# Performance work log

Hardware: AMD Instinct MI355X
Metric: run time of the kernel (lower is better)

## Reference

```python
import jax, jax.numpy as jnp
import numpy as np

DIM, HEADS, DFF = 768, 12, 3072
DK = DIM // HEADS
EPS = 1e-5

def _layernorm(x, w, b):
    mu = jnp.mean(x, axis=-1, keepdims=True)
    var = jnp.mean(jnp.square(x - mu), axis=-1, keepdims=True)
    return (x - mu) * jax.lax.rsqrt(var + EPS) * w + b

def setup_inputs() -> dict:
    key = jax.random.key(0)
    ks = jax.random.split(key, 5)
    B, N = 8, 1024
    std = 0.02
    return {
        "x": jax.random.normal(ks[0], (B, N, DIM), jnp.float32),
        "ln1_w": jnp.ones((DIM,), jnp.float32),
        "ln1_b": jnp.zeros((DIM,), jnp.float32),
        "qkv_w": jax.random.normal(ks[1], (3 * DIM, DIM), jnp.float32) * std,
        "qkv_b": jnp.zeros((3 * DIM,), jnp.float32),
        "proj_w": jax.random.normal(ks[2], (DIM, DIM), jnp.float32) * std,
        "proj_b": jnp.zeros((DIM,), jnp.float32),
        "ln2_w": jnp.ones((DIM,), jnp.float32),
        "ln2_b": jnp.zeros((DIM,), jnp.float32),
        "fc1_w": jax.random.normal(ks[3], (DFF, DIM), jnp.float32) * std,
        "fc1_b": jnp.zeros((DFF,), jnp.float32),
        "fc2_w": jax.random.normal(ks[4], (DIM, DFF), jnp.float32) * std,
        "fc2_b": jnp.zeros((DIM,), jnp.float32),
    }

def reference(x, ln1_w, ln1_b, qkv_w, qkv_b, proj_w, proj_b,
              ln2_w, ln2_b, fc1_w, fc1_b, fc2_w, fc2_b):
    B, N, C = x.shape
    # --- attention branch (pre-norm) ---
    h = _layernorm(x, ln1_w, ln1_b)
    qkv = h @ qkv_w.T + qkv_b                      # [B,N,3C]
    qkv = qkv.reshape(B, N, 3, HEADS, DK)
    q = qkv[:, :, 0].transpose(0, 2, 1, 3)         # [B,H,N,dk]
    k = qkv[:, :, 1].transpose(0, 2, 1, 3)
    v = qkv[:, :, 2].transpose(0, 2, 1, 3)
    scale = DK ** -0.5
    attn = jnp.einsum('bhnd,bhmd->bhnm', q, k) * scale
    attn = jax.nn.softmax(attn, axis=-1)
    out = jnp.einsum('bhnm,bhmd->bhnd', attn, v)   # [B,H,N,dk]
    out = out.transpose(0, 2, 1, 3).reshape(B, N, C)
    out = out @ proj_w.T + proj_b
    x = x + out
    # --- MLP branch (pre-norm) ---
    h = _layernorm(x, ln2_w, ln2_b)
    h = jax.nn.gelu(h @ fc1_w.T + fc1_b, approximate=False)
    h = h @ fc2_w.T + fc2_b
    return x + h
```

## Files before the change

kernel.cpp:

```cpp
#include <hip/hip_runtime.h>
#include <hip/hip_bf16.h>
#include <hip/hip_fp8.h>
#include <math.h>

typedef __attribute__((ext_vector_type(8))) __bf16 bf16x8;
typedef __attribute__((ext_vector_type(4))) __bf16 bf16x4;
typedef __attribute__((ext_vector_type(4))) float f32x4;
typedef __attribute__((ext_vector_type(4))) int i32x4;
typedef __attribute__((ext_vector_type(8))) int i32x8;

#define DIM 768
#define DFF 3072
#define HEADS 12
#define DKH 64
#define SEQ 1024
#define BATCH 8
#define ROWS (SEQ * BATCH)

#define GLD16(gp, lp)                                                      \
  __builtin_amdgcn_global_load_lds(                                        \
      (const __attribute__((address_space(1))) void*)(gp),                 \
      (__attribute__((address_space(3))) void*)(lp), 16, 0, 0)

__device__ __forceinline__ unsigned int pack4_e4m3(float a, float b, float c, float d) {
  __hip_fp8_e4m3 q0(a), q1(b), q2(c), q3(d);
  return (unsigned int)q0.__x | ((unsigned int)q1.__x << 8) |
         ((unsigned int)q2.__x << 16) | ((unsigned int)q3.__x << 24);
}

__global__ __launch_bounds__(256) void cvt4_kernel(const float* __restrict__ s0, int n0,
                                                   const float* __restrict__ s1, int n1,
                                                   const float* __restrict__ s2, int n2,
                                                   const float* __restrict__ s3, int n3,
                                                   __bf16* __restrict__ d0,
                                                   __bf16* __restrict__ d1,
                                                   unsigned char* __restrict__ d2,
                                                   unsigned char* __restrict__ d3) {
  int i0 = blockIdx.x * 256 + threadIdx.x;
  int st = gridDim.x * 256;
  const float* bsrc[2] = {s0, s1};
  __bf16* bdst[2] = {d0, d1};
  int bns[2] = {n0, n1};
#pragma unroll
  for (int t = 0; t < 2; ++t) {
    const f32x4* in = reinterpret_cast<const f32x4*>(bsrc[t]);
    bf16x4* out = reinterpret_cast<bf16x4*>(bdst[t]);
    for (int i = i0; i < bns[t]; i += st) {
      f32x4 v = in[i];
      bf16x4 o;
#pragma unroll
      for (int j = 0; j < 4; ++j) o[j] = (__bf16)v[j];
      out[i] = o;
    }
  }
  const float* fsrc[2] = {s2, s3};
  unsigned char* fdst[2] = {d2, d3};
  int fns[2] = {n2, n3};
#pragma unroll
  for (int t = 0; t < 2; ++t) {
    const f32x4* in = reinterpret_cast<const f32x4*>(fsrc[t]);
    unsigned int* out = reinterpret_cast<unsigned int*>(fdst[t]);
    for (int i = i0; i < fns[t]; i += st) {
      f32x4 v = in[i];
      out[i] = pack4_e4m3(v[0] * 16.f, v[1] * 16.f, v[2] * 16.f, v[3] * 16.f);
    }
  }
}

__global__ __launch_bounds__(256) void ln_kernel(const float* __restrict__ x,
                                                 const float* __restrict__ w,
                                                 const float* __restrict__ b,
                                                 __bf16* __restrict__ out) {
  int wid = threadIdx.x >> 6, lane = threadIdx.x & 63;
  int row = blockIdx.x * 4 + wid;
  const f32x4* xp = reinterpret_cast<const f32x4*>(x + (size_t)row * DIM);
  f32x4 v[3];
  float s1 = 0.f, s2 = 0.f;
#pragma unroll
  for (int i = 0; i < 3; ++i) {
    v[i] = xp[lane + i * 64];
#pragma unroll
    for (int c = 0; c < 4; ++c) { s1 += v[i][c]; s2 += v[i][c] * v[i][c]; }
  }
#pragma unroll
  for (int off = 1; off < 64; off <<= 1) {
    s1 += __shfl_xor(s1, off, 64);
    s2 += __shfl_xor(s2, off, 64);
  }
  float mu = s1 * (1.f / DIM);
  float var = s2 * (1.f / DIM) - mu * mu;
  float rs = rsqrtf(var + 1e-5f);
  const f32x4* wp = reinterpret_cast<const f32x4*>(w);
  const f32x4* bp = reinterpret_cast<const f32x4*>(b);
  __bf16* op = out + (size_t)row * DIM;
#pragma unroll
  for (int i = 0; i < 3; ++i) {
    int c4 = lane + i * 64;
    f32x4 wv = wp[c4], bv = bp[c4];
    bf16x4 ov;
#pragma unroll
    for (int c = 0; c < 4; ++c) ov[c] = (__bf16)((v[i][c] - mu) * rs * wv[c] + bv[c]);
    *reinterpret_cast<bf16x4*>(&op[c4 * 4]) = ov;
  }
}

__global__ __launch_bounds__(256) void ln_f8_kernel(const float* __restrict__ x,
                                                    const float* __restrict__ w,
                                                    const float* __restrict__ b,
                                                    unsigned char* __restrict__ out) {
  int wid = threadIdx.x >> 6, lane = threadIdx.x & 63;
  int row = blockIdx.x * 4 + wid;
  const f32x4* xp = reinterpret_cast<const f32x4*>(x + (size_t)row * DIM);
  f32x4 v[3];
  float s1 = 0.f, s2 = 0.f;
#pragma unroll
  for (int i = 0; i < 3; ++i) {
    v[i] = xp[lane + i * 64];
#pragma unroll
    for (int c = 0; c < 4; ++c) { s1 += v[i][c]; s2 += v[i][c] * v[i][c]; }
  }
#pragma unroll
  for (int off = 1; off < 64; off <<= 1) {
    s1 += __shfl_xor(s1, off, 64);
    s2 += __shfl_xor(s2, off, 64);
  }
  float mu = s1 * (1.f / DIM);
  float var = s2 * (1.f / DIM) - mu * mu;
  float rs = rsqrtf(var + 1e-5f);
  const f32x4* wp = reinterpret_cast<const f32x4*>(w);
  const f32x4* bp = reinterpret_cast<const f32x4*>(b);
  unsigned int* op = reinterpret_cast<unsigned int*>(out + (size_t)row * DIM);
#pragma unroll
  for (int i = 0; i < 3; ++i) {
    int c4 = lane + i * 64;
    f32x4 wv = wp[c4], bv = bp[c4];
    float o0 = (v[i][0] - mu) * rs * wv[0] + bv[0];
    float o1 = (v[i][1] - mu) * rs * wv[1] + bv[1];
    float o2 = (v[i][2] - mu) * rs * wv[2] + bv[2];
    float o3 = (v[i][3] - mu) * rs * wv[3] + bv[3];
    op[c4] = pack4_e4m3(o0, o1, o2, o3);
  }
}

template <int EPI, int BN, int DBUF>
__global__ __launch_bounds__(256, 3) void gemm_nt(const __bf16* __restrict__ A,
                                                  const __bf16* __restrict__ B,
                                                  const float* __restrict__ bias,
                                                  const float* __restrict__ resid,
                                                  __bf16* __restrict__ vt,
                                                  void* __restrict__ Cout,
                                                  int M, int N, int K) {
  constexpr int NBUF = DBUF ? 2 : 1;
  constexpr int MF = (BN == 128) ? 4 : 2;
  static_assert(BN == 64, "vmcnt count assumes 6 staging loads per thread");
  __shared__ __bf16 As[NBUF * 128 * 64];
  __shared__ __bf16 Bs[NBUF * BN * 64];
  int tid = threadIdx.x;
  int bm = blockIdx.x, bn = blockIdx.y;
  int wid = tid >> 6, lane = tid & 63;
  int l15 = lane & 15, l4 = lane >> 4;
  int rowb = (BN == 128) ? (wid >> 1) * 64 : wid * 32;
  int colb = (BN == 128) ? (wid & 1) * 64 : 0;

  f32x4 acc[MF][4] = {};

  auto stage = [&](int buf, int kt) {
    __bf16* Ab = As + buf * 128 * 64;
    __bf16* Bb = Bs + buf * BN * 64;
#pragma unroll
    for (int r = 0; r < 4; ++r) {
      int c0 = (r * 4 + wid) * 64;
      int c = c0 + lane;
      int row = c >> 3;
      int colE = ((c & 7) ^ (row & 7)) * 8;
      GLD16(&A[(size_t)(bm * 128 + row) * K + kt + colE], &Ab[c0 * 8]);
    }
#pragma unroll
    for (int r = 0; r < BN / 32; ++r) {
      int c0 = (r * 4 + wid) * 64;
      int c = c0 + lane;
      int row = c >> 3;
      int colE = ((c & 7) ^ (row & 7)) * 8;
      GLD16(&B[(size_t)(bn * BN + row) * K + kt + colE], &Bb[c0 * 8]);
    }
  };

  auto compute = [&](int buf) {
    const __bf16* Ab = As + buf * 128 * 64;
    const __bf16* Bb = Bs + buf * BN * 64;
#pragma unroll
    for (int kc = 0; kc < 2; ++kc) {
      int cswz = ((kc * 4 + l4) ^ (l15 & 7)) * 8;
      bf16x8 af[MF], bfr[4];
#pragma unroll
      for (int m = 0; m < MF; ++m)
        af[m] = *reinterpret_cast<const bf16x8*>(&Ab[(rowb + m * 16 + l15) * 64 + cswz]);
#pragma unroll
      for (int n = 0; n < 4; ++n)
        bfr[n] = *reinterpret_cast<const bf16x8*>(&Bb[(colb + n * 16 + l15) * 64 + cswz]);
#pragma unroll
      for (int m = 0; m < MF; ++m)
#pragma unroll
        for (int n = 0; n < 4; ++n)
          acc[m][n] = __builtin_amdgcn_mfma_f32_16x16x32_bf16(af[m], bfr[n], acc[m][n], 0, 0, 0);
    }
  };

  if constexpr (DBUF) {
    stage(0, 0);
    int cur = 0;
    for (int kt = 0; kt < K; kt += 64) {
      if (kt + 64 < K) {
        stage(cur ^ 1, kt + 64);
        asm volatile("s_waitcnt vmcnt(6)" ::: "memory");
      } else {
        asm volatile("s_waitcnt vmcnt(0)" ::: "memory");
      }
      __builtin_amdgcn_s_barrier();
      compute(cur);
      asm volatile("s_waitcnt lgkmcnt(0)" ::: "memory");
      __builtin_amdgcn_s_barrier();
      cur ^= 1;
    }
  } else {
    for (int kt = 0; kt < K; kt += 64) {
      __syncthreads();
      stage(0, kt);
      __syncthreads();
      compute(0);
    }
  }

#pragma unroll
  for (int m = 0; m < MF; ++m)
#pragma unroll
    for (int n = 0; n < 4; ++n) {
      int row0 = bm * 128 + rowb + m * 16 + l4 * 4;
      int col = bn * BN + colb + n * 16 + l15;
      float bc = bias[col];
      if (EPI == 0 && col >= 2 * DIM) {
        int h = (col - 2 * DIM) >> 6, dk = (col - 2 * DIM) & 63;
        int b = row0 >> 10, tok = row0 & 1023;
        bf16x4 pk;
#pragma unroll
        for (int j = 0; j < 4; ++j) pk[j] = (__bf16)(acc[m][n][j] + bc);
        *reinterpret_cast<bf16x4*>(
            &vt[(size_t)((b * HEADS + h) * DKH + dk) * SEQ + tok]) = pk;
      } else {
#pragma unroll
        for (int j = 0; j < 4; ++j) {
          float v = acc[m][n][j] + bc;
          size_t idx = (size_t)(row0 + j) * N + col;
          if (EPI == 0) {
            ((__bf16*)Cout)[idx] = (__bf16)v;
          } else {
            ((float*)Cout)[idx] = v + resid[idx];
          }
        }
      }
    }
}

template <int EPI>
__global__ __launch_bounds__(256, 3) void gemm_fp8(const unsigned char* __restrict__ A,
                                                   const unsigned char* __restrict__ B,
                                                   const float* __restrict__ bias,
                                                   const float* __restrict__ resid,
                                                   void* __restrict__ Cout,
                                                   int M, int N, int K) {
  __shared__ unsigned char As[2 * 128 * 128];
  __shared__ unsigned char Bs[2 * 64 * 128];
  int tid = threadIdx.x;
  int bm = blockIdx.x, bn = blockIdx.y;
  int wid = tid >> 6, lane = tid & 63;
  int l15 = lane & 15, l4 = lane >> 4;
  int rowb = wid * 32;

  f32x4 acc[2][4] = {};

  auto stage = [&](int buf, int kt) {
    unsigned char* Ab = As + buf * 128 * 128;
    unsigned char* Bb = Bs + buf * 64 * 128;
#pragma unroll
    for (int r = 0; r < 4; ++r) {
      int c0 = (r * 4 + wid) * 64;
      int c = c0 + lane;
      int row = c >> 3;
      int j = (c & 7) ^ (row & 7);
      GLD16(&A[(size_t)(bm * 128 + row) * K + kt + j * 16], &Ab[c0 * 16]);
    }
#pragma unroll
    for (int r = 0; r < 2; ++r) {
      int c0 = (r * 4 + wid) * 64;
      int c = c0 + lane;
      int row = c >> 3;
      int j = (c & 7) ^ (row & 7);
      GLD16(&B[(size_t)(bn * 64 + row) * K + kt + j * 16], &Bb[c0 * 16]);
    }
  };

  auto ld32 = [&](const unsigned char* base, int row) -> i32x8 {
    int s7 = l15 & 7;
    i32x8 r;
    *reinterpret_cast<i32x4*>(&r) =
        *reinterpret_cast<const i32x4*>(&base[row * 128 + (((2 * l4) ^ s7) * 16)]);
    *(reinterpret_cast<i32x4*>(&r) + 1) =
        *reinterpret_cast<const i32x4*>(&base[row * 128 + (((2 * l4 + 1) ^ s7) * 16)]);
    return r;
  };

  auto compute = [&](int buf) {
    const unsigned char* Ab = As + buf * 128 * 128;
    const unsigned char* Bb = Bs + buf * 64 * 128;
    i32x8 af[2], bfr[4];
#pragma unroll
    for (int m = 0; m < 2; ++m) af[m] = ld32(Ab, rowb + m * 16 + l15);
#pragma unroll
    for (int n = 0; n < 4; ++n) bfr[n] = ld32(Bb, n * 16 + l15);
#pragma unroll
    for (int m = 0; m < 2; ++m)
#pragma unroll
      for (int n = 0; n < 4; ++n)
        acc[m][n] = __builtin_amdgcn_mfma_scale_f32_16x16x128_f8f6f4(
            af[m], bfr[n], acc[m][n], 0, 0,
            0, 0x7F7F7F7F,
            0, 0x7F7F7F7F);
  };

  stage(0, 0);
  int cur = 0;
  for (int kt = 0; kt < K; kt += 128) {
    if (kt + 128 < K) {
      stage(cur ^ 1, kt + 128);
      asm volatile("s_waitcnt vmcnt(6)" ::: "memory");
    } else {
      asm volatile("s_waitcnt vmcnt(0)" ::: "memory");
    }
    __builtin_amdgcn_s_barrier();
    compute(cur);
    asm volatile("s_waitcnt lgkmcnt(0)" ::: "memory");
    __builtin_amdgcn_s_barrier();
    cur ^= 1;
  }

#pragma unroll
  for (int m = 0; m < 2; ++m)
#pragma unroll
    for (int n = 0; n < 4; ++n) {
      int row0 = bm * 128 + rowb + m * 16 + l4 * 4;
      int col = bn * 64 + n * 16 + l15;
      float bc = bias[col];
#pragma unroll
      for (int j = 0; j < 4; ++j) {
        if (EPI == 0) {
          float v = acc[m][n][j] * 0.0625f + bc;
          float z = 1.59576912f * (v + 0.044715f * v * v * v);
          float tt = __expf(fminf(z, 80.f));
          float g = v * __fdividef(tt, tt + 1.0f);
          ((unsigned char*)Cout)[(size_t)(row0 + j) * N + col] =
              __hip_fp8_e4m3(g * 16.f).__x;
        } else {
          size_t idx = (size_t)(row0 + j) * N + col;
          ((float*)Cout)[idx] = acc[m][n][j] * (1.f / 256.f) + bc + resid[idx];
        }
      }
    }
}

__global__ __launch_bounds__(256, 3) void attn_kernel(const __bf16* __restrict__ qkv,
                                                      const __bf16* __restrict__ vt,
                                                      __bf16* __restrict__ out) {
  int bid = blockIdx.x;
  int xcd = bid & 7, kk0 = bid >> 3;
  int bh = (kk0 >> 3) * 8 + xcd;
  int qt = kk0 & 7;
  int b = bh / HEADS, h = bh % HEADS;
  int tid = threadIdx.x, wid = tid >> 6, lane = tid & 63;
  int l15 = lane & 15, l4 = lane >> 4;
  int qr0 = qt * 128 + wid * 32;
  const size_t rs = 3 * DIM;
  const __bf16* Qb = qkv + (size_t)(b * SEQ) * rs + h * DKH;
  const __bf16* Kb = Qb + DIM;
  const __bf16* Vb = vt + (size_t)bh * DKH * SEQ;

  __shared__ __bf16 Ks[64 * 64];
  __shared__ __bf16 Vs[64 * 64];
  __shared__ __bf16 Ps[4][32][72];
  __bf16(*Psw)[72] = Ps[wid];

  bf16x8 qf[2][2];
#pragma unroll
  for (int m = 0; m < 2; ++m)
#pragma unroll
    for (int kc = 0; kc < 2; ++kc) {
      bf16x8 t = *reinterpret_cast<const bf16x8*>(
          &Qb[(size_t)(qr0 + m * 16 + l15) * rs + kc * 32 + l4 * 8]);
#pragma unroll
      for (int e = 0; e < 8; ++e) t[e] = (__bf16)((float)t[e] * 0.125f);
      qf[m][kc] = t;
    }

  f32x4 o[2][4] = {};
  f32x4 lsum[2] = {};

  for (int kv0 = 0; kv0 < SEQ; kv0 += 64) {
    __syncthreads();
#pragma unroll
    for (int cc = 0; cc < 2; ++cc) {
      int c0 = (wid * 2 + cc) * 64;
      int c = c0 + lane;
      int row = c >> 3;
      int sb = (c & 7) * 16;
      int pkc = sb ^ (((row >> 2) & 7) << 4);
      GLD16(&Kb[(size_t)(kv0 + row) * rs + (pkc >> 1)], &Ks[c0 * 8]);
      int pvc = sb ^ ((row & 7) << 4);
      GLD16(&Vb[(size_t)row * SEQ + kv0 + (pvc >> 1)], &Vs[c0 * 8]);
    }
    __syncthreads();

    bf16x8 kb[4][2];
#pragma unroll
    for (int nf = 0; nf < 4; ++nf)
#pragma unroll
      for (int kc = 0; kc < 2; ++kc) {
        int row = 4 * l15 + nf;
        int col = (kc * 64 + l4 * 16) ^ ((l15 & 7) << 4);
        kb[nf][kc] = *reinterpret_cast<const bf16x8*>(&Ks[row * 64 + (col >> 1)]);
      }
    f32x4 s[2][4] = {};
#pragma unroll
    for (int m = 0; m < 2; ++m)
#pragma unroll
      for (int nf = 0; nf < 4; ++nf)
#pragma unroll
        for (int kc = 0; kc < 2; ++kc)
          s[m][nf] = __builtin_amdgcn_mfma_f32_16x16x32_bf16(qf[m][kc], kb[nf][kc], s[m][nf], 0, 0, 0);

    bf16x8 vf[4][2];
#pragma unroll
    for (int d = 0; d < 4; ++d)
#pragma unroll
      for (int kc = 0; kc < 2; ++kc) {
        int row = d * 16 + l15;
        int col = (kc * 64 + l4 * 16) ^ ((l15 & 7) << 4);
        vf[d][kc] = *reinterpret_cast<const bf16x8*>(&Vs[row * 64 + (col >> 1)]);
      }

#pragma unroll
    for (int m = 0; m < 2; ++m)
#pragma unroll
      for (int j = 0; j < 4; ++j) {
        bf16x4 pk;
        float ss = 0.f;
#pragma unroll
        for (int nf = 0; nf < 4; ++nf) {
          float p = __expf(s[m][nf][j]);
          ss += p;
          pk[nf] = (__bf16)p;
        }
        lsum[m][j] += ss;
        *reinterpret_cast<bf16x4*>(&Psw[m * 16 + l4 * 4 + j][l15 * 4]) = pk;
      }
    asm volatile("s_waitcnt lgkmcnt(0)" ::: "memory");
    __builtin_amdgcn_sched_barrier(0);

    bf16x8 pf[2][2];
#pragma unroll
    for (int m = 0; m < 2; ++m)
#pragma unroll
      for (int kc = 0; kc < 2; ++kc)
        pf[m][kc] = *reinterpret_cast<const bf16x8*>(&Psw[m * 16 + l15][kc * 32 + l4 * 8]);
#pragma unroll
    for (int m = 0; m < 2; ++m)
#pragma unroll
      for (int d = 0; d < 4; ++d)
#pragma unroll
        for (int kc = 0; kc < 2; ++kc)
          o[m][d] = __builtin_amdgcn_mfma_f32_16x16x32_bf16(pf[m][kc], vf[d][kc], o[m][d], 0, 0, 0);
  }

#pragma unroll
  for (int off = 1; off < 16; off <<= 1)
#pragma unroll
    for (int m = 0; m < 2; ++m)
#pragma unroll
      for (int j = 0; j < 4; ++j) lsum[m][j] += __shfl_xor(lsum[m][j], off, 64);

  __bf16* op = out + (size_t)(b * SEQ) * DIM + h * DKH;
#pragma unroll
  for (int m = 0; m < 2; ++m)
#pragma unroll
    for (int j = 0; j < 4; ++j) {
      float rl = 1.f / lsum[m][j];
      int row = qr0 + m * 16 + l4 * 4 + j;
#pragma unroll
      for (int d = 0; d < 4; ++d)
        op[(size_t)row * DIM + d * 16 + l15] = (__bf16)(o[m][d][j] * rl);
    }
}

extern "C" void kernel_launch(void* const* d_in, const int* in_sizes, int n_in,
                              void* d_out, int out_size, void* d_ws, size_t ws_size,
                              hipStream_t stream) {
  const float* x      = (const float*)d_in[0];
  const float* ln1_w  = (const float*)d_in[1];
  const float* ln1_b  = (const float*)d_in[2];
  const float* qkv_w  = (const float*)d_in[3];
  const float* qkv_b  = (const float*)d_in[4];
  const float* proj_w = (const float*)d_in[5];
  const float* proj_b = (const float*)d_in[6];
  const float* ln2_w  = (const float*)d_in[7];
  const float* ln2_b  = (const float*)d_in[8];
  const float* fc1_w  = (const float*)d_in[9];
  const float* fc1_b  = (const float*)d_in[10];
  const float* fc2_w  = (const float*)d_in[11];
  const float* fc2_b  = (const float*)d_in[12];

  char* ws = (char*)d_ws;
  size_t o = 0;
  __bf16* qkvw_bf = (__bf16*)(ws + o); o += (size_t)3 * DIM * DIM * 2;
  __bf16* projw_bf = (__bf16*)(ws + o); o += (size_t)DIM * DIM * 2;
  unsigned char* fc1w_f8 = (unsigned char*)(ws + o); o += (size_t)DFF * DIM;
  unsigned char* fc2w_f8 = (unsigned char*)(ws + o); o += (size_t)DIM * DFF;
  __bf16* h_bf    = (__bf16*)(ws + o); o += (size_t)ROWS * DIM * 2;
  float*  x1      = (float*)(ws + o);  o += (size_t)ROWS * DIM * 4;
  __bf16* qkv_bf  = (__bf16*)(ws + o); o += (size_t)ROWS * 3 * DIM * 2;
  __bf16* attn_bf = (__bf16*)(ws + o); o += (size_t)ROWS * DIM * 2;
  unsigned char* ff_f8 = (unsigned char*)qkv_bf;
  __bf16* vtp     = (__bf16*)x1;
  unsigned char* h_f8 = (unsigned char*)h_bf;

  cvt4_kernel<<<2048, 256, 0, stream>>>(
      qkv_w, 3 * DIM * DIM / 4, proj_w, DIM * DIM / 4,
      fc1_w, DFF * DIM / 4, fc2_w, DIM * DFF / 4,
      qkvw_bf, projw_bf, fc1w_f8, fc2w_f8);

  ln_kernel<<<ROWS / 4, 256, 0, stream>>>(x, ln1_w, ln1_b, h_bf);
  gemm_nt<0, 64, 1><<<dim3(ROWS / 128, 3 * DIM / 64), 256, 0, stream>>>(
      h_bf, qkvw_bf, qkv_b, nullptr, vtp, qkv_bf, ROWS, 3 * DIM, DIM);
  attn_kernel<<<dim3(8 * BATCH * HEADS), 256, 0, stream>>>(qkv_bf, vtp, attn_bf);
  gemm_nt<2, 64, 1><<<dim3(ROWS / 128, DIM / 64), 256, 0, stream>>>(
      attn_bf, projw_bf, proj_b, x, nullptr, x1, ROWS, DIM, DIM);
  ln_f8_kernel<<<ROWS / 4, 256, 0, stream>>>(x1, ln2_w, ln2_b, h_f8);
  gemm_fp8<0><<<dim3(ROWS / 128, DFF / 64), 256, 0, stream>>>(
      h_f8, fc1w_f8, fc1_b, nullptr, ff_f8, ROWS, DFF, DIM);
  gemm_fp8<1><<<dim3(ROWS / 128, DIM / 64), 256, 0, stream>>>(
      ff_f8, fc2w_f8, fc2_b, x1, (float*)d_out, ROWS, DIM, DFF);
}
```

Measured before the change: 193.5 us.

## Widen GEMM tiles to 128x128 with 8 waves per block

```diff
diff --git a/kernel.cpp b/kernel.cpp
--- a/kernel.cpp
+++ b/kernel.cpp
@@ -142,101 +142,89 @@
   }
 }
 
-template <int EPI, int BN, int DBUF>
-__global__ __launch_bounds__(256, 3) void gemm_nt(const __bf16* __restrict__ A,
+template <int EPI>
+__global__ __launch_bounds__(512, 4) void gemm_nt(const __bf16* __restrict__ A,
                                                   const __bf16* __restrict__ B,
                                                   const float* __restrict__ bias,
                                                   const float* __restrict__ resid,
                                                   __bf16* __restrict__ vt,
                                                   void* __restrict__ Cout,
                                                   int M, int N, int K) {
-  constexpr int NBUF = DBUF ? 2 : 1;
-  constexpr int MF = (BN == 128) ? 4 : 2;
-  static_assert(BN == 64, "vmcnt count assumes 6 staging loads per thread");
-  __shared__ __bf16 As[NBUF * 128 * 64];
-  __shared__ __bf16 Bs[NBUF * BN * 64];
+  __shared__ __bf16 As[2 * 128 * 64];
+  __shared__ __bf16 Bs[2 * 128 * 64];
   int tid = threadIdx.x;
   int bm = blockIdx.x, bn = blockIdx.y;
   int wid = tid >> 6, lane = tid & 63;
   int l15 = lane & 15, l4 = lane >> 4;
-  int rowb = (BN == 128) ? (wid >> 1) * 64 : wid * 32;
-  int colb = (BN == 128) ? (wid & 1) * 64 : 0;
-
-  f32x4 acc[MF][4] = {};
+  int rowb = (wid >> 1) * 32;
+  int colb = (wid & 1) * 64;
+
+  f32x4 acc[2][4] = {};
 
   auto stage = [&](int buf, int kt) {
     __bf16* Ab = As + buf * 128 * 64;
-    __bf16* Bb = Bs + buf * BN * 64;
-#pragma unroll
-    for (int r = 0; r < 4; ++r) {
-      int c0 = (r * 4 + wid) * 64;
+    __bf16* Bb = Bs + buf * 128 * 64;
+#pragma unroll
+    for (int r = 0; r < 2; ++r) {
+      int c0 = (r * 8 + wid) * 64;
       int c = c0 + lane;
       int row = c >> 3;
       int colE = ((c & 7) ^ (row & 7)) * 8;
       GLD16(&A[(size_t)(bm * 128 + row) * K + kt + colE], &Ab[c0 * 8]);
     }
 #pragma unroll
-    for (int r = 0; r < BN / 32; ++r) {
-      int c0 = (r * 4 + wid) * 64;
+    for (int r = 0; r < 2; ++r) {
+      int c0 = (r * 8 + wid) * 64;
       int c = c0 + lane;
       int row = c >> 3;
       int colE = ((c & 7) ^ (row & 7)) * 8;
-      GLD16(&B[(size_t)(bn * BN + row) * K + kt + colE], &Bb[c0 * 8]);
+      GLD16(&B[(size_t)(bn * 128 + row) * K + kt + colE], &Bb[c0 * 8]);
     }
   };
 
   auto compute = [&](int buf) {
     const __bf16* Ab = As + buf * 128 * 64;
-    const __bf16* Bb = Bs + buf * BN * 64;
+    const __bf16* Bb = Bs + buf * 128 * 64;
 #pragma unroll
     for (int kc = 0; kc < 2; ++kc) {
       int cswz = ((kc * 4 + l4) ^ (l15 & 7)) * 8;
-      bf16x8 af[MF], bfr[4];
-#pragma unroll
-      for (int m = 0; m < MF; ++m)
+      bf16x8 af[2], bfr[4];
+#pragma unroll
+      for (int m = 0; m < 2; ++m)
         af[m] = *reinterpret_cast<const bf16x8*>(&Ab[(rowb + m * 16 + l15) * 64 + cswz]);
 #pragma unroll
       for (int n = 0; n < 4; ++n)
         bfr[n] = *reinterpret_cast<const bf16x8*>(&Bb[(colb + n * 16 + l15) * 64 + cswz]);
 #pragma unroll
-      for (int m = 0; m < MF; ++m)
+      for (int m = 0; m < 2; ++m)
 #pragma unroll
         for (int n = 0; n < 4; ++n)
           acc[m][n] = __builtin_amdgcn_mfma_f32_16x16x32_bf16(af[m], bfr[n], acc[m][n], 0, 0, 0);
     }
   };
 
-  if constexpr (DBUF) {
-    stage(0, 0);
-    int cur = 0;
-    for (int kt = 0; kt < K; kt += 64) {
-      if (kt + 64 < K) {
-        stage(cur ^ 1, kt + 64);
-        asm volatile("s_waitcnt vmcnt(6)" ::: "memory");
-      } else {
-        asm volatile("s_waitcnt vmcnt(0)" ::: "memory");
-      }
-      __builtin_amdgcn_s_barrier();
-      compute(cur);
-      asm volatile("s_waitcnt lgkmcnt(0)" ::: "memory");
-      __builtin_amdgcn_s_barrier();
-      cur ^= 1;
-    }
-  } else {
-    for (int kt = 0; kt < K; kt += 64) {
-      __syncthreads();
-      stage(0, kt);
-      __syncthreads();
-      compute(0);
-    }
-  }
-
-#pragma unroll
-  for (int m = 0; m < MF; ++m)
+  stage(0, 0);
+  int cur = 0;
+  for (int kt = 0; kt < K; kt += 64) {
+    if (kt + 64 < K) {
+      stage(cur ^ 1, kt + 64);
+      asm volatile("s_waitcnt vmcnt(4)" ::: "memory");
+    } else {
+      asm volatile("s_waitcnt vmcnt(0)" ::: "memory");
+    }
+    __builtin_amdgcn_s_barrier();
+    compute(cur);
+    asm volatile("s_waitcnt lgkmcnt(0)" ::: "memory");
+    __builtin_amdgcn_s_barrier();
+    cur ^= 1;
+  }
+
+#pragma unroll
+  for (int m = 0; m < 2; ++m)
 #pragma unroll
     for (int n = 0; n < 4; ++n) {
       int row0 = bm * 128 + rowb + m * 16 + l4 * 4;
-      int col = bn * BN + colb + n * 16 + l15;
+      int col = bn * 128 + colb + n * 16 + l15;
       float bc = bias[col];
       if (EPI == 0 && col >= 2 * DIM) {
         int h = (col - 2 * DIM) >> 6, dk = (col - 2 * DIM) & 63;
@@ -262,28 +250,29 @@
 }
 
 template <int EPI>
-__global__ __launch_bounds__(256, 3) void gemm_fp8(const unsigned char* __restrict__ A,
+__global__ __launch_bounds__(512, 4) void gemm_fp8(const unsigned char* __restrict__ A,
                                                    const unsigned char* __restrict__ B,
                                                    const float* __restrict__ bias,
                                                    const float* __restrict__ resid,
                                                    void* __restrict__ Cout,
                                                    int M, int N, int K) {
   __shared__ unsigned char As[2 * 128 * 128];
-  __shared__ unsigned char Bs[2 * 64 * 128];
+  __shared__ unsigned char Bs[2 * 128 * 128];
   int tid = threadIdx.x;
   int bm = blockIdx.x, bn = blockIdx.y;
   int wid = tid >> 6, lane = tid & 63;
   int l15 = lane & 15, l4 = lane >> 4;
-  int rowb = wid * 32;
+  int rowb = (wid >> 1) * 32;
+  int colb = (wid & 1) * 64;
 
   f32x4 acc[2][4] = {};
 
   auto stage = [&](int buf, int kt) {
     unsigned char* Ab = As + buf * 128 * 128;
-    unsigned char* Bb = Bs + buf * 64 * 128;
-#pragma unroll
-    for (int r = 0; r < 4; ++r) {
-      int c0 = (r * 4 + wid) * 64;
+    unsigned char* Bb = Bs + buf * 128 * 128;
+#pragma unroll
+    for (int r = 0; r < 2; ++r) {
+      int c0 = (r * 8 + wid) * 64;
       int c = c0 + lane;
       int row = c >> 3;
       int j = (c & 7) ^ (row & 7);
@@ -291,11 +280,11 @@
     }
 #pragma unroll
     for (int r = 0; r < 2; ++r) {
-      int c0 = (r * 4 + wid) * 64;
+      int c0 = (r * 8 + wid) * 64;
       int c = c0 + lane;
       int row = c >> 3;
       int j = (c & 7) ^ (row & 7);
-      GLD16(&B[(size_t)(bn * 64 + row) * K + kt + j * 16], &Bb[c0 * 16]);
+      GLD16(&B[(size_t)(bn * 128 + row) * K + kt + j * 16], &Bb[c0 * 16]);
     }
   };
 
@@ -311,12 +300,12 @@
 
   auto compute = [&](int buf) {
     const unsigned char* Ab = As + buf * 128 * 128;
-    const unsigned char* Bb = Bs + buf * 64 * 128;
+    const unsigned char* Bb = Bs + buf * 128 * 128;
     i32x8 af[2], bfr[4];
 #pragma unroll
     for (int m = 0; m < 2; ++m) af[m] = ld32(Ab, rowb + m * 16 + l15);
 #pragma unroll
-    for (int n = 0; n < 4; ++n) bfr[n] = ld32(Bb, n * 16 + l15);
+    for (int n = 0; n < 4; ++n) bfr[n] = ld32(Bb, colb + n * 16 + l15);
 #pragma unroll
     for (int m = 0; m < 2; ++m)
 #pragma unroll
@@ -332,7 +321,7 @@
   for (int kt = 0; kt < K; kt += 128) {
     if (kt + 128 < K) {
       stage(cur ^ 1, kt + 128);
-      asm volatile("s_waitcnt vmcnt(6)" ::: "memory");
+      asm volatile("s_waitcnt vmcnt(4)" ::: "memory");
     } else {
       asm volatile("s_waitcnt vmcnt(0)" ::: "memory");
     }
@@ -348,7 +337,7 @@
 #pragma unroll
     for (int n = 0; n < 4; ++n) {
       int row0 = bm * 128 + rowb + m * 16 + l4 * 4;
-      int col = bn * 64 + n * 16 + l15;
+      int col = bn * 128 + colb + n * 16 + l15;
       float bc = bias[col];
 #pragma unroll
       for (int j = 0; j < 4; ++j) {
@@ -536,14 +525,14 @@
       qkvw_bf, projw_bf, fc1w_f8, fc2w_f8);
 
   ln_kernel<<<ROWS / 4, 256, 0, stream>>>(x, ln1_w, ln1_b, h_bf);
-  gemm_nt<0, 64, 1><<<dim3(ROWS / 128, 3 * DIM / 64), 256, 0, stream>>>(
+  gemm_nt<0><<<dim3(ROWS / 128, 3 * DIM / 128), 512, 0, stream>>>(
       h_bf, qkvw_bf, qkv_b, nullptr, vtp, qkv_bf, ROWS, 3 * DIM, DIM);
   attn_kernel<<<dim3(8 * BATCH * HEADS), 256, 0, stream>>>(qkv_bf, vtp, attn_bf);
-  gemm_nt<2, 64, 1><<<dim3(ROWS / 128, DIM / 64), 256, 0, stream>>>(
+  gemm_nt<2><<<dim3(ROWS / 128, DIM / 128), 512, 0, stream>>>(
       attn_bf, projw_bf, proj_b, x, nullptr, x1, ROWS, DIM, DIM);
   ln_f8_kernel<<<ROWS / 4, 256, 0, stream>>>(x1, ln2_w, ln2_b, h_f8);
-  gemm_fp8<0><<<dim3(ROWS / 128, DFF / 64), 256, 0, stream>>>(
+  gemm_fp8<0><<<dim3(ROWS / 128, DFF / 128), 512, 0, stream>>>(
       h_f8, fc1w_f8, fc1_b, nullptr, ff_f8, ROWS, DFF, DIM);
-  gemm_fp8<1><<<dim3(ROWS / 128, DIM / 64), 256, 0, stream>>>(
+  gemm_fp8<1><<<dim3(ROWS / 128, DIM / 128), 512, 0, stream>>>(
       ff_f8, fc2w_f8, fc2_b, x1, (float*)d_out, ROWS, DIM, DFF);
 }
```

New measurement: 192.3 us. Within noise of the previous version (-0.6%).

## Drop double-buffered LDS staging in GEMMs to raise occupancy to four blocks

Applied to the files above, without the earlier changes.

```diff
diff --git a/kernel.cpp b/kernel.cpp
--- a/kernel.cpp
+++ b/kernel.cpp
@@ -143,7 +143,7 @@
 }
 
 template <int EPI, int BN, int DBUF>
-__global__ __launch_bounds__(256, 3) void gemm_nt(const __bf16* __restrict__ A,
+__global__ __launch_bounds__(256, 4) void gemm_nt(const __bf16* __restrict__ A,
                                                   const __bf16* __restrict__ B,
                                                   const float* __restrict__ bias,
                                                   const float* __restrict__ resid,
@@ -152,15 +152,15 @@
                                                   int M, int N, int K) {
   constexpr int NBUF = DBUF ? 2 : 1;
   constexpr int MF = (BN == 128) ? 4 : 2;
-  static_assert(BN == 64, "vmcnt count assumes 6 staging loads per thread");
+  static_assert(BN == 64, "geometry assumes BN=64");
   __shared__ __bf16 As[NBUF * 128 * 64];
   __shared__ __bf16 Bs[NBUF * BN * 64];
   int tid = threadIdx.x;
   int bm = blockIdx.x, bn = blockIdx.y;
   int wid = tid >> 6, lane = tid & 63;
   int l15 = lane & 15, l4 = lane >> 4;
-  int rowb = (BN == 128) ? (wid >> 1) * 64 : wid * 32;
-  int colb = (BN == 128) ? (wid & 1) * 64 : 0;
+  int rowb = wid * 32;
+  int colb = 0;
 
   f32x4 acc[MF][4] = {};
 
@@ -262,14 +262,14 @@
 }
 
 template <int EPI>
-__global__ __launch_bounds__(256, 3) void gemm_fp8(const unsigned char* __restrict__ A,
+__global__ __launch_bounds__(256, 4) void gemm_fp8(const unsigned char* __restrict__ A,
                                                    const unsigned char* __restrict__ B,
                                                    const float* __restrict__ bias,
                                                    const float* __restrict__ resid,
                                                    void* __restrict__ Cout,
                                                    int M, int N, int K) {
-  __shared__ unsigned char As[2 * 128 * 128];
-  __shared__ unsigned char Bs[2 * 64 * 128];
+  __shared__ unsigned char As[128 * 128];
+  __shared__ unsigned char Bs[64 * 128];
   int tid = threadIdx.x;
   int bm = blockIdx.x, bn = blockIdx.y;
   int wid = tid >> 6, lane = tid & 63;
@@ -278,16 +278,14 @@
 
   f32x4 acc[2][4] = {};
 
-  auto stage = [&](int buf, int kt) {
-    unsigned char* Ab = As + buf * 128 * 128;
-    unsigned char* Bb = Bs + buf * 64 * 128;
+  auto stage = [&](int kt) {
 #pragma unroll
     for (int r = 0; r < 4; ++r) {
       int c0 = (r * 4 + wid) * 64;
       int c = c0 + lane;
       int row = c >> 3;
       int j = (c & 7) ^ (row & 7);
-      GLD16(&A[(size_t)(bm * 128 + row) * K + kt + j * 16], &Ab[c0 * 16]);
+      GLD16(&A[(size_t)(bm * 128 + row) * K + kt + j * 16], &As[c0 * 16]);
     }
 #pragma unroll
     for (int r = 0; r < 2; ++r) {
@@ -295,7 +293,7 @@
       int c = c0 + lane;
       int row = c >> 3;
       int j = (c & 7) ^ (row & 7);
-      GLD16(&B[(size_t)(bn * 64 + row) * K + kt + j * 16], &Bb[c0 * 16]);
+      GLD16(&B[(size_t)(bn * 64 + row) * K + kt + j * 16], &Bs[c0 * 16]);
     }
   };
 
@@ -309,14 +307,12 @@
     return r;
   };
 
-  auto compute = [&](int buf) {
-    const unsigned char* Ab = As + buf * 128 * 128;
-    const unsigned char* Bb = Bs + buf * 64 * 128;
+  auto compute = [&]() {
     i32x8 af[2], bfr[4];
 #pragma unroll
-    for (int m = 0; m < 2; ++m) af[m] = ld32(Ab, rowb + m * 16 + l15);
-#pragma unroll
-    for (int n = 0; n < 4; ++n) bfr[n] = ld32(Bb, n * 16 + l15);
+    for (int m = 0; m < 2; ++m) af[m] = ld32(As, rowb + m * 16 + l15);
+#pragma unroll
+    for (int n = 0; n < 4; ++n) bfr[n] = ld32(Bs, n * 16 + l15);
 #pragma unroll
     for (int m = 0; m < 2; ++m)
 #pragma unroll
@@ -327,20 +323,11 @@
             0, 0x7F7F7F7F);
   };
 
-  stage(0, 0);
-  int cur = 0;
   for (int kt = 0; kt < K; kt += 128) {
-    if (kt + 128 < K) {
-      stage(cur ^ 1, kt + 128);
-      asm volatile("s_waitcnt vmcnt(6)" ::: "memory");
-    } else {
-      asm volatile("s_waitcnt vmcnt(0)" ::: "memory");
-    }
-    __builtin_amdgcn_s_barrier();
-    compute(cur);
-    asm volatile("s_waitcnt lgkmcnt(0)" ::: "memory");
-    __builtin_amdgcn_s_barrier();
-    cur ^= 1;
+    __syncthreads();
+    stage(kt);
+    __syncthreads();
+    compute();
   }
 
 #pragma unroll
@@ -536,10 +523,10 @@
       qkvw_bf, projw_bf, fc1w_f8, fc2w_f8);
 
   ln_kernel<<<ROWS / 4, 256, 0, stream>>>(x, ln1_w, ln1_b, h_bf);
-  gemm_nt<0, 64, 1><<<dim3(ROWS / 128, 3 * DIM / 64), 256, 0, stream>>>(
+  gemm_nt<0, 64, 0><<<dim3(ROWS / 128, 3 * DIM / 64), 256, 0, stream>>>(
       h_bf, qkvw_bf, qkv_b, nullptr, vtp, qkv_bf, ROWS, 3 * DIM, DIM);
   attn_kernel<<<dim3(8 * BATCH * HEADS), 256, 0, stream>>>(qkv_bf, vtp, attn_bf);
-  gemm_nt<2, 64, 1><<<dim3(ROWS / 128, DIM / 64), 256, 0, stream>>>(
+  gemm_nt<2, 64, 0><<<dim3(ROWS / 128, DIM / 64), 256, 0, stream>>>(
       attn_bf, projw_bf, proj_b, x, nullptr, x1, ROWS, DIM, DIM);
   ln_f8_kernel<<<ROWS / 4, 256, 0, stream>>>(x1, ln2_w, ln2_b, h_f8);
   gemm_fp8<0><<<dim3(ROWS / 128, DFF / 64), 256, 0, stream>>>(
```

New measurement: 183.4 us (median of 2 runs). 5.2% less time.
